# Kernel optimization log

Measured on AMD Instinct MI355X. Metric: run time of the kernel, lower is better.

Reference implementation:

```python
import jax, jax.numpy as jnp
import numpy as np
import math

D_MODEL = 512
HEADS = 8
GRID_COUNT = 40000
MAX_LEN = 5000


def _positional_embedding(d_model, max_len=MAX_LEN):
    pe = np.zeros((max_len, d_model), dtype=np.float32)
    position = np.arange(max_len, dtype=np.float32)[:, None]
    div_term = np.exp(np.arange(0, d_model, 2, dtype=np.float32) * -(math.log(10000.0) / d_model))
    pe[:, 0::2] = np.sin(position * div_term)
    pe[:, 1::2] = np.cos(position * div_term)
    return jnp.asarray(pe)  # [max_len, d_model]


def _mha(q, k, v, wq, bq, wk, bk, wv, bv, heads):
    # Faithful to SelfAttention: no 1/sqrt(d_k) scaling in the original.
    B, Sq, D = q.shape
    Sk = k.shape[1]
    dh = D // heads
    Q = (q @ wq.T + bq).reshape(B, Sq, heads, dh)
    K = (k @ wk.T + bk).reshape(B, Sk, heads, dh)
    V = (v @ wv.T + bv).reshape(B, Sk, heads, dh)
    attn = jax.nn.softmax(jnp.einsum('bqhd,bkhd->bhqk', Q, K), axis=-1)
    out = jnp.einsum('bhqk,bkhd->bqhd', attn, V)
    return out.reshape(B, Sq, D)


def setup_inputs() -> dict:
    key = jax.random.key(0)
    ks = jax.random.split(key, 20)
    B, S_CURR, S_HIST, N_MASK = 32, 128, 256, 16
    s = 1.0 / math.sqrt(D_MODEL)

    def lin(k):
        kw, kb = jax.random.split(k)
        w = jax.random.uniform(kw, (D_MODEL, D_MODEL), jnp.float32, -s, s)
        b = jax.random.uniform(kb, (D_MODEL,), jnp.float32, -s, s)
        return w, b

    h_wq, h_bq = lin(ks[0]); h_wk, h_bk = lin(ks[1]); h_wv, h_bv = lin(ks[2])
    c_wq, c_bq = lin(ks[3]); c_wk, c_bk = lin(ks[4]); c_wv, c_bv = lin(ks[5])
    x_wq, x_bq = lin(ks[6]); x_wk, x_bk = lin(ks[7]); x_wv, x_bv = lin(ks[8])
    t2_w, t2_b = lin(ks[9])
    emb = jax.random.normal(ks[10], (GRID_COUNT, D_MODEL), jnp.float32)

    return {
        'hist_traj_grid': jax.random.randint(ks[11], (B, S_HIST), 0, GRID_COUNT),
        'userId': jax.random.randint(ks[12], (B,), 0, 1000),
        'mask_pos': jax.random.randint(ks[13], (B, N_MASK), 0, S_CURR),
        'mask_curr_traj_grid': jax.random.randint(ks[14], (B, S_CURR), 0, GRID_COUNT),
        'aggregator_hist_traj_grid': jax.random.randint(ks[15], (B, S_HIST), 0, GRID_COUNT),
        'emb': emb,
        'h_wq': h_wq, 'h_bq': h_bq, 'h_wk': h_wk, 'h_bk': h_bk, 'h_wv': h_wv, 'h_bv': h_bv,
        'c_wq': c_wq, 'c_bq': c_bq, 'c_wk': c_wk, 'c_bk': c_bk, 'c_wv': c_wv, 'c_bv': c_bv,
        'x_wq': x_wq, 'x_bq': x_bq, 'x_wk': x_wk, 'x_bk': x_bk, 'x_wv': x_wv, 'x_bv': x_bv,
        't2_w': t2_w, 't2_b': t2_b,
    }


def reference(hist_traj_grid, userId, mask_pos, mask_curr_traj_grid, aggregator_hist_traj_grid,
              emb,
              h_wq, h_bq, h_wk, h_bk, h_wv, h_bv,
              c_wq, c_bq, c_wk, c_bk, c_wv, c_bv,
              x_wq, x_bq, x_wk, x_bk, x_wv, x_bv,
              t2_w, t2_b):
    pe = _positional_embedding(D_MODEL)
    hist = emb[aggregator_hist_traj_grid]          # [B, S_hist, D]
    curr = emb[mask_curr_traj_grid]                # [B, S_curr, D]
    hist = hist + pe[None, :hist.shape[1]]
    curr = curr + pe[None, :curr.shape[1]]

    hist = _mha(hist, hist, hist, h_wq, h_bq, h_wk, h_bk, h_wv, h_bv, HEADS)
    curr = _mha(curr, curr, curr, c_wq, c_bq, c_wk, c_bk, c_wv, c_bv, HEADS)
    _cross = _mha(curr, hist, hist, x_wq, x_bq, x_wk, x_bk, x_wv, x_bv, HEADS)
    # NOTE: original overwrites liner_transform output with liner_transform2(tanh(curr)),
    # so cross-attention output and liner_transform do not affect the result.
    hyb = jnp.tanh(curr) @ t2_w.T + t2_b           # [B, S_curr, D]

    # index_select of flattened [B*S, D] at mask_pos + b*S == take_along_axis over seq dim
    gathered = jnp.take_along_axis(hyb, mask_pos[:, :, None], axis=1)  # [B, n_mask, D]
    gathered = gathered.reshape(-1, D_MODEL)

    candidate = emb[2:]                            # [vocab-2, D]
    scores = gathered @ candidate.T                # [B*n_mask, vocab-2]
    return jax.nn.log_softmax(scores, axis=-1)
```

## Files before the change

kernel.cpp:

```cpp
#include <hip/hip_runtime.h>
#include <hip/hip_bf16.h>
#include <math.h>
#include <float.h>

#define B       32
#define S_CURR  128
#define D       512
#define H       8
#define DH      64
#define NM      16
#define NCAND   39998
#define MG      (B * NM)
#define SCLD    40064
#define NT      313

typedef __bf16 bf16x8_t __attribute__((ext_vector_type(8)));
typedef float  f32x4_t  __attribute__((ext_vector_type(4)));

typedef __attribute__((address_space(3))) unsigned int lds_u32_t;
typedef const __attribute__((address_space(1))) unsigned int gbl_u32_t;

__device__ __forceinline__ void async16(const void* g, void* l) {
    __builtin_amdgcn_global_load_lds((gbl_u32_t*)g, (lds_u32_t*)l, 16, 0, 0);
}

__global__ __launch_bounds__(256) void prep_kernel(
    const float* __restrict__ emb,
    const float* __restrict__ wq, const float* __restrict__ wk,
    const float* __restrict__ wv, const float* __restrict__ t2w,
    __bf16* __restrict__ embB, __bf16* __restrict__ wqB, __bf16* __restrict__ wkB,
    __bf16* __restrict__ wvB, __bf16* __restrict__ t2wB,
    const int* __restrict__ curr_idx, __bf16* __restrict__ currB,
    const int* __restrict__ mask_pos, int* __restrict__ qidx)
{
    int bx = blockIdx.x;
    if (bx < 10512) {
        const float* src; __bf16* dst; size_t n, base;
        if (bx < 10000) {
            src = emb + 2 * D; dst = embB; n = (size_t)NCAND * D; base = (size_t)bx * 2048;
        } else {
            int w = (bx - 10000) >> 7;
            base = (size_t)((bx - 10000) & 127) * 2048;
            n = (size_t)D * D;
            src = (w == 0) ? wq : (w == 1) ? wk : (w == 2) ? wv : t2w;
            dst = (w == 0) ? wqB : (w == 1) ? wkB : (w == 2) ? wvB : t2wB;
        }
        size_t i = base + (size_t)threadIdx.x * 8;
        if (i >= n) return;
        float4 a = *(const float4*)(src + i);
        float4 b = *(const float4*)(src + i + 4);
        bf16x8_t v;
        v[0] = (__bf16)a.x; v[1] = (__bf16)a.y; v[2] = (__bf16)a.z; v[3] = (__bf16)a.w;
        v[4] = (__bf16)b.x; v[5] = (__bf16)b.y; v[6] = (__bf16)b.z; v[7] = (__bf16)b.w;
        *(bf16x8_t*)(dst + i) = v;
        return;
    }
    if (bx == 14608) {
        int r = threadIdx.x;
        qidx[r] = (r >> 4) * S_CURR + mask_pos[r];
        r += 256;
        qidx[r] = (r >> 4) * S_CURR + mask_pos[r];
        return;
    }
    int bs = bx - 10512;
    int s = bs & (S_CURR - 1);
    int g = curr_idx[bs];
    const float* e = emb + (size_t)g * D;
    __bf16* o = currB + (size_t)bs * D;
    int d = threadIdx.x * 2;
    float div = expf(-(float)d * (9.210340371976184f / 512.0f));
    float ang = (float)s * div;
    o[d]     = (__bf16)(e[d]     + sinf(ang));
    o[d + 1] = (__bf16)(e[d + 1] + cosf(ang));
}

__global__ __launch_bounds__(256) void gemm_bf(
    const __bf16* __restrict__ A,
    const __bf16* __restrict__ W0, const float* __restrict__ b0, __bf16* __restrict__ C0,
    const __bf16* __restrict__ W1, const float* __restrict__ b1, __bf16* __restrict__ C1,
    const __bf16* __restrict__ W2, const float* __restrict__ b2, __bf16* __restrict__ C2,
    const int* __restrict__ rowidx)
{
    const int z = blockIdx.z;
    if (z == 2 && blockIdx.x >= 4) return;
    const __bf16* W = (z == 0) ? W0 : (z == 1) ? W1 : W2;
    const float* bias = (z == 0) ? b0 : (z == 1) ? b1 : b2;
    __bf16* C = (z == 0) ? C0 : (z == 1) ? C1 : C2;

    __shared__ __bf16 As[128 * 64];
    __shared__ __bf16 Bs[128 * 64];

    const int tid = threadIdx.x, lane = tid & 63, wave = tid >> 6;
    const int wy = wave >> 1, wx = wave & 1;
    const int m0 = blockIdx.x * 128, n0 = blockIdx.y * 128;
    const int lrow = lane >> 3;
    const int lcol = (((lane & 7) ^ lrow) & 7) * 8;

    const __bf16* aptr[4]; const __bf16* bptr[4];
#pragma unroll
    for (int i = 0; i < 4; ++i) {
        int chunk = wave * 4 + i;
        int ar = m0 + chunk * 8 + lrow;
        if (z == 2) ar = rowidx[ar];
        aptr[i] = A + (size_t)ar * 512 + lcol;
        bptr[i] = W + (size_t)(n0 + chunk * 8 + lrow) * 512 + lcol;
    }

    f32x4_t acc[4][4];
#pragma unroll
    for (int i = 0; i < 4; ++i)
#pragma unroll
        for (int j = 0; j < 4; ++j) acc[i][j] = (f32x4_t){0.f, 0.f, 0.f, 0.f};

    const int l7 = lane & 7, quad = lane >> 4, c16 = lane & 15;

    for (int kk = 0; kk < 512; kk += 64) {
#pragma unroll
        for (int i = 0; i < 4; ++i) {
            int chunk = wave * 4 + i;
            async16(aptr[i] + kk, &As[chunk * 512]);
            async16(bptr[i] + kk, &Bs[chunk * 512]);
        }
        __syncthreads();
#pragma unroll
        for (int kb = 0; kb < 2; ++kb) {
            const int goff = (((kb * 4 + quad) ^ l7)) * 8;
            bf16x8_t af[4], bfv[4];
#pragma unroll
            for (int i = 0; i < 4; ++i)
                af[i] = *(const bf16x8_t*)&As[(wy * 64 + i * 16 + c16) * 64 + goff];
#pragma unroll
            for (int j = 0; j < 4; ++j)
                bfv[j] = *(const bf16x8_t*)&Bs[(wx * 64 + j * 16 + c16) * 64 + goff];
#pragma unroll
            for (int i = 0; i < 4; ++i)
#pragma unroll
                for (int j = 0; j < 4; ++j)
                    acc[i][j] = __builtin_amdgcn_mfma_f32_16x16x32_bf16(
                        af[i], bfv[j], acc[i][j], 0, 0, 0);
        }
        __syncthreads();
    }

#pragma unroll
    for (int i = 0; i < 4; ++i)
#pragma unroll
        for (int j = 0; j < 4; ++j) {
            int col = n0 + wx * 64 + j * 16 + c16;
            float bv = bias[col];
#pragma unroll
            for (int rr = 0; rr < 4; ++rr) {
                int row = m0 + wy * 64 + i * 16 + quad * 4 + rr;
                C[(size_t)row * 512 + col] = (__bf16)(acc[i][j][rr] + bv);
            }
        }
}

__global__ __launch_bounds__(256) void gemm_scores(
    const __bf16* __restrict__ A,
    const __bf16* __restrict__ Bm,
    __bf16* __restrict__ scB,
    float* __restrict__ pmax, float* __restrict__ psum)
{
    const int bid = blockIdx.x;
    const int xcd = bid & 7, k = bid >> 3;
    const int nt = xcd * 40 + (k >> 2);
    if (nt >= NT) return;
    const int m0 = (k & 3) * 128, n0 = nt * 128;

    __shared__ __bf16 As[128 * 64];
    __shared__ __bf16 Bs[128 * 64];
    __shared__ float redm[2][128], reds[2][128];

    const int tid = threadIdx.x, lane = tid & 63, wave = tid >> 6;
    const int wy = wave >> 1, wx = wave & 1;
    const int lrow = lane >> 3;
    const int lcol = (((lane & 7) ^ lrow) & 7) * 8;

    const __bf16* aptr[4]; const __bf16* bptr[4];
#pragma unroll
    for (int i = 0; i < 4; ++i) {
        int chunk = wave * 4 + i;
        aptr[i] = A + (size_t)(m0 + chunk * 8 + lrow) * 512 + lcol;
        bptr[i] = Bm + (size_t)(n0 + chunk * 8 + lrow) * 512 + lcol;
    }

    f32x4_t acc[4][4];
#pragma unroll
    for (int i = 0; i < 4; ++i)
#pragma unroll
        for (int j = 0; j < 4; ++j) acc[i][j] = (f32x4_t){0.f, 0.f, 0.f, 0.f};

    const int l7 = lane & 7, quad = lane >> 4, c16 = lane & 15;

    for (int kk = 0; kk < 512; kk += 64) {
#pragma unroll
        for (int i = 0; i < 4; ++i) {
            int chunk = wave * 4 + i;
            async16(aptr[i] + kk, &As[chunk * 512]);
            async16(bptr[i] + kk, &Bs[chunk * 512]);
        }
        __syncthreads();
#pragma unroll
        for (int kb = 0; kb < 2; ++kb) {
            const int goff = (((kb * 4 + quad) ^ l7)) * 8;
            bf16x8_t af[4], bfv[4];
#pragma unroll
            for (int i = 0; i < 4; ++i)
                af[i] = *(const bf16x8_t*)&As[(wy * 64 + i * 16 + c16) * 64 + goff];
#pragma unroll
            for (int j = 0; j < 4; ++j)
                bfv[j] = *(const bf16x8_t*)&Bs[(wx * 64 + j * 16 + c16) * 64 + goff];
#pragma unroll
            for (int i = 0; i < 4; ++i)
#pragma unroll
                for (int j = 0; j < 4; ++j)
                    acc[i][j] = __builtin_amdgcn_mfma_f32_16x16x32_bf16(
                        af[i], bfv[j], acc[i][j], 0, 0, 0);
        }
        __syncthreads();
    }

#pragma unroll
    for (int i = 0; i < 4; ++i) {
#pragma unroll
        for (int rr = 0; rr < 4; ++rr) {
            const int row = wy * 64 + i * 16 + quad * 4 + rr;
            const size_t rowbase = (size_t)(m0 + row) * SCLD;
            float v[4]; float m = -FLT_MAX;
#pragma unroll
            for (int j = 0; j < 4; ++j) {
                int col = n0 + wx * 64 + j * 16 + c16;
                __bf16 xb = (__bf16)acc[i][j][rr];
                if (col < NCAND) {
                    scB[rowbase + col] = xb;
                    float xr = (float)xb;
                    v[j] = xr; m = fmaxf(m, xr);
                } else v[j] = -FLT_MAX;
            }
            float s = 0.f;
#pragma unroll
            for (int j = 0; j < 4; ++j)
                s += (v[j] > -FLT_MAX) ? __expf(v[j] - m) : 0.f;
#pragma unroll
            for (int mk = 1; mk < 16; mk <<= 1) {
                float om = __shfl_xor(m, mk);
                float os = __shfl_xor(s, mk);
                float mm = fmaxf(m, om);
                s = s * __expf(m - mm) + os * __expf(om - mm);
                m = mm;
            }
            if (c16 == 0) { redm[wx][row] = m; reds[wx][row] = s; }
        }
    }
    __syncthreads();
    if (tid < 128) {
        float ma = redm[0][tid], sa = reds[0][tid];
        float mb = redm[1][tid], sb = reds[1][tid];
        float mm = fmaxf(ma, mb);
        float ss = sa * __expf(ma - mm) + sb * __expf(mb - mm);
        pmax[(size_t)nt * MG + m0 + tid] = mm;
        psum[(size_t)nt * MG + m0 + tid] = ss;
    }
}

#define KPAD 72
__global__ __launch_bounds__(256) void attn_kernel(const __bf16* __restrict__ Qg,
                                                   const __bf16* __restrict__ K,
                                                   const __bf16* __restrict__ V,
                                                   __bf16* __restrict__ attnB) {
    const int b = blockIdx.x, h = blockIdx.y, t = threadIdx.x;
    __shared__ __bf16 Ks[128 * KPAD];
    __shared__ __bf16 Vs[128 * KPAD];
    __shared__ float  Qs[16 * 68];
    __shared__ float  P[16 * 130];

    for (int i = t; i < 1024; i += 256) {
        int row = i >> 3, cg = (i & 7) * 8;
        size_t gsrc = ((size_t)(b * S_CURR + row)) * D + h * DH + cg;
        *(bf16x8_t*)&Ks[row * KPAD + cg] = *(const bf16x8_t*)&K[gsrc];
        *(bf16x8_t*)&Vs[row * KPAD + cg] = *(const bf16x8_t*)&V[gsrc];
    }
    if (t < 128) {
        int q = t >> 3, cg = (t & 7) * 8;
        bf16x8_t qv = *(const bf16x8_t*)&Qg[((size_t)(b * NM + q)) * D + h * DH + cg];
#pragma unroll
        for (int u = 0; u < 8; ++u) Qs[q * 68 + cg + u] = (float)qv[u];
    }
    __syncthreads();

    const int q = t >> 4, i = t & 15;
    float sv[8];
    float lmax = -FLT_MAX;
#pragma unroll
    for (int z = 0; z < 8; ++z) {
        int kk = i + z * 16;
        float s = 0.f;
#pragma unroll
        for (int d0 = 0; d0 < DH; d0 += 8) {
            bf16x8_t kv = *(const bf16x8_t*)&Ks[kk * KPAD + d0];
#pragma unroll
            for (int u = 0; u < 8; ++u) s += Qs[q * 68 + d0 + u] * (float)kv[u];
        }
        sv[z] = s; lmax = fmaxf(lmax, s);
    }
#pragma unroll
    for (int mk = 1; mk < 16; mk <<= 1) lmax = fmaxf(lmax, __shfl_xor(lmax, mk));
    float lsum = 0.f;
#pragma unroll
    for (int z = 0; z < 8; ++z) {
        float e = __expf(sv[z] - lmax);
        P[q * 130 + i + z * 16] = e;
        lsum += e;
    }
#pragma unroll
    for (int mk = 1; mk < 16; mk <<= 1) lsum += __shfl_xor(lsum, mk);
    const float inv = 1.0f / lsum;

    const int d = i * 4;
    float a0 = 0.f, a1 = 0.f, a2 = 0.f, a3 = 0.f;
    for (int kk = 0; kk < 128; ++kk) {
        float p = P[q * 130 + kk];
        const __bf16* vr = &Vs[kk * KPAD + d];
        a0 += p * (float)vr[0]; a1 += p * (float)vr[1];
        a2 += p * (float)vr[2]; a3 += p * (float)vr[3];
    }
    __bf16* o = attnB + ((size_t)(b * NM + q)) * D + h * DH + d;
    o[0] = (__bf16)tanhf(a0 * inv); o[1] = (__bf16)tanhf(a1 * inv);
    o[2] = (__bf16)tanhf(a2 * inv); o[3] = (__bf16)tanhf(a3 * inv);
}

__global__ __launch_bounds__(256) void lse_reduce(const float* __restrict__ pmax,
                                                  const float* __restrict__ psum,
                                                  float* __restrict__ lse) {
    int row = blockIdx.x, t = threadIdx.x;
    float m = -FLT_MAX, s = 0.f;
    for (int i = t; i < NT; i += 256) {
        float om = pmax[(size_t)i * MG + row];
        float os = psum[(size_t)i * MG + row];
        float mm = fmaxf(m, om);
        s = s * __expf(m - mm) + os * __expf(om - mm);
        m = mm;
    }
    __shared__ float ms[256], ss[256];
    ms[t] = m; ss[t] = s;
    __syncthreads();
    for (int off = 128; off > 0; off >>= 1) {
        if (t < off) {
            float m1 = ms[t], s1 = ss[t], m2 = ms[t + off], s2 = ss[t + off];
            float mm = fmaxf(m1, m2);
            ms[t] = mm;
            ss[t] = s1 * __expf(m1 - mm) + s2 * __expf(m2 - mm);
        }
        __syncthreads();
    }
    if (t == 0) lse[row] = ms[0] + logf(ss[0]);
}

__global__ __launch_bounds__(256) void final_out(const __bf16* __restrict__ scB,
                                                 const float* __restrict__ lse,
                                                 float* __restrict__ out) {
    int row = blockIdx.y;
    int c0 = (blockIdx.x * 256 + threadIdx.x) * 8;
    if (c0 >= NCAND) return;
    float l = lse[row];
    bf16x8_t v = *(const bf16x8_t*)(scB + (size_t)row * SCLD + c0);
    float* o = out + (size_t)row * NCAND + c0;
    if (c0 + 8 <= NCAND) {
        *(float2*)(o)     = make_float2((float)v[0] - l, (float)v[1] - l);
        *(float2*)(o + 2) = make_float2((float)v[2] - l, (float)v[3] - l);
        *(float2*)(o + 4) = make_float2((float)v[4] - l, (float)v[5] - l);
        *(float2*)(o + 6) = make_float2((float)v[6] - l, (float)v[7] - l);
    } else {
        for (int k2 = 0; k2 < NCAND - c0; ++k2) o[k2] = (float)v[k2] - l;
    }
}

extern "C" void kernel_launch(void* const* d_in, const int* in_sizes, int n_in,
                              void* d_out, int out_size, void* d_ws, size_t ws_size,
                              hipStream_t stream) {
    const int*   mask_pos = (const int*)d_in[2];
    const int*   curr_idx = (const int*)d_in[3];
    const float* emb      = (const float*)d_in[5];
    const float* c_wq = (const float*)d_in[12];
    const float* c_bq = (const float*)d_in[13];
    const float* c_wk = (const float*)d_in[14];
    const float* c_bk = (const float*)d_in[15];
    const float* c_wv = (const float*)d_in[16];
    const float* c_bv = (const float*)d_in[17];
    const float* t2_w = (const float*)d_in[24];
    const float* t2_b = (const float*)d_in[25];
    float* out = (float*)d_out;

    char* w = (char*)d_ws;
    __bf16* embB  = (__bf16*)w;
    __bf16* scB   = (__bf16*)(w + 41025536);
    __bf16* currB = scB;
    __bf16* Kf    = (__bf16*)(w + 41025536 + 4194304);
    __bf16* Vf    = (__bf16*)(w + 41025536 + 8388608);
    __bf16* Qg    = (__bf16*)(w + 41025536 + 12582912);
    __bf16* attnB = (__bf16*)(w + 41025536 + 13107200);
    __bf16* wqB   = (__bf16*)(w + 41025536 + 13631488);
    __bf16* wkB   = (__bf16*)(w + 41025536 + 14155776);
    __bf16* wvB   = (__bf16*)(w + 41025536 + 14680064);
    __bf16* t2wB  = (__bf16*)(w + 41025536 + 15204352);
    int*    qidx  = (int*)   (w + 41025536 + 15728640);
    __bf16* gatheredB = (__bf16*)(w + 82051072);
    float*  pmax  = (float*)(w + 82575360);
    float*  psum  = (float*)(w + 83216384);
    float*  lse   = (float*)(w + 83857408);

    hipLaunchKernelGGL(prep_kernel, dim3(14609), dim3(256), 0, stream,
                       emb, c_wq, c_wk, c_wv, t2_w, embB, wqB, wkB, wvB, t2wB,
                       curr_idx, currB, mask_pos, qidx);
    hipLaunchKernelGGL(gemm_bf, dim3(32, 4, 3), dim3(256), 0, stream,
                       currB, wkB, c_bk, Kf, wvB, c_bv, Vf, wqB, c_bq, Qg, qidx);
    hipLaunchKernelGGL(attn_kernel, dim3(B, H), dim3(256), 0, stream,
                       Qg, Kf, Vf, attnB);
    hipLaunchKernelGGL(gemm_bf, dim3(4, 4, 1), dim3(256), 0, stream,
                       attnB, t2wB, t2_b, gatheredB,
                       t2wB, t2_b, gatheredB, t2wB, t2_b, gatheredB,
                       (const int*)nullptr);
    hipLaunchKernelGGL(gemm_scores, dim3(1280), dim3(256), 0, stream,
                       gatheredB, embB, scB, pmax, psum);
    hipLaunchKernelGGL(lse_reduce, dim3(MG), dim3(256), 0, stream, pmax, psum, lse);
    hipLaunchKernelGGL(final_out, dim3(20, MG), dim3(256), 0, stream, scB, lse, out);
}
```

Measured before the change: 305.6 us.

## Double-buffer GEMM LDS tiles and widen scores tile to 128x256

Both GEMM kernels now use two LDS buffers. The next K-slice is prefetched with async global-to-LDS loads while MFMAs run on the current slice, meant to hide global load latency behind compute. The scores GEMM also grows its output tile from 128x128 to 128x256, which halves the number of column tiles and the per-tile partial max/sum entries that lse_reduce has to combine. Its in-tile softmax reduction is simplified to a max-reduce followed by a sum-reduce. The trade-off is more LDS per block, more accumulator registers (launch_bounds now asks for occupancy 1) and fewer blocks to spread across the GPU.

Result: slower. 334.6 us (+9.5%).

```diff
diff --git a/kernel.cpp b/kernel.cpp
--- a/kernel.cpp
+++ b/kernel.cpp
@@ -12,7 +12,7 @@
 #define NCAND   39998
 #define MG      (B * NM)
 #define SCLD    40064
-#define NT      313
+#define NT2     157
 
 typedef __bf16 bf16x8_t __attribute__((ext_vector_type(8)));
 typedef float  f32x4_t  __attribute__((ext_vector_type(4)));
@@ -87,8 +87,8 @@
     const float* bias = (z == 0) ? b0 : (z == 1) ? b1 : b2;
     __bf16* C = (z == 0) ? C0 : (z == 1) ? C1 : C2;
 
-    __shared__ __bf16 As[128 * 64];
-    __shared__ __bf16 Bs[128 * 64];
+    __shared__ __bf16 As[2][128 * 64];
+    __shared__ __bf16 Bs[2][128 * 64];
 
     const int tid = threadIdx.x, lane = tid & 63, wave = tid >> 6;
     const int wy = wave >> 1, wx = wave & 1;
@@ -114,24 +114,35 @@
 
     const int l7 = lane & 7, quad = lane >> 4, c16 = lane & 15;
 
-    for (int kk = 0; kk < 512; kk += 64) {
-#pragma unroll
-        for (int i = 0; i < 4; ++i) {
-            int chunk = wave * 4 + i;
-            async16(aptr[i] + kk, &As[chunk * 512]);
-            async16(bptr[i] + kk, &Bs[chunk * 512]);
-        }
-        __syncthreads();
+#pragma unroll
+    for (int i = 0; i < 4; ++i) {
+        int chunk = wave * 4 + i;
+        async16(aptr[i], &As[0][chunk * 512]);
+        async16(bptr[i], &Bs[0][chunk * 512]);
+    }
+    __syncthreads();
+
+    for (int it = 0; it < 8; ++it) {
+        const int cur = it & 1;
+        if (it < 7) {
+            const int kk = (it + 1) * 64;
+#pragma unroll
+            for (int i = 0; i < 4; ++i) {
+                int chunk = wave * 4 + i;
+                async16(aptr[i] + kk, &As[cur ^ 1][chunk * 512]);
+                async16(bptr[i] + kk, &Bs[cur ^ 1][chunk * 512]);
+            }
+        }
 #pragma unroll
         for (int kb = 0; kb < 2; ++kb) {
-            const int goff = (((kb * 4 + quad) ^ l7)) * 8;
+            const int goff = ((kb * 4 + quad) ^ l7) * 8;
             bf16x8_t af[4], bfv[4];
 #pragma unroll
             for (int i = 0; i < 4; ++i)
-                af[i] = *(const bf16x8_t*)&As[(wy * 64 + i * 16 + c16) * 64 + goff];
+                af[i] = *(const bf16x8_t*)&As[cur][(wy * 64 + i * 16 + c16) * 64 + goff];
 #pragma unroll
             for (int j = 0; j < 4; ++j)
-                bfv[j] = *(const bf16x8_t*)&Bs[(wx * 64 + j * 16 + c16) * 64 + goff];
+                bfv[j] = *(const bf16x8_t*)&Bs[cur][(wx * 64 + j * 16 + c16) * 64 + goff];
 #pragma unroll
             for (int i = 0; i < 4; ++i)
 #pragma unroll
@@ -156,7 +167,7 @@
         }
 }
 
-__global__ __launch_bounds__(256) void gemm_scores(
+__global__ __launch_bounds__(256, 1) void gemm_scores(
     const __bf16* __restrict__ A,
     const __bf16* __restrict__ Bm,
     __bf16* __restrict__ scB,
@@ -164,57 +175,66 @@
 {
     const int bid = blockIdx.x;
     const int xcd = bid & 7, k = bid >> 3;
-    const int nt = xcd * 40 + (k >> 2);
-    if (nt >= NT) return;
-    const int m0 = (k & 3) * 128, n0 = nt * 128;
-
-    __shared__ __bf16 As[128 * 64];
-    __shared__ __bf16 Bs[128 * 64];
+    const int n2 = xcd * 20 + (k >> 2);
+    if (n2 >= NT2) return;
+    const int m0 = (k & 3) * 128, n0 = n2 * 256;
+
+    __shared__ __bf16 As[2][128 * 64];
+    __shared__ __bf16 Bs[2][256 * 64];
     __shared__ float redm[2][128], reds[2][128];
 
     const int tid = threadIdx.x, lane = tid & 63, wave = tid >> 6;
-    const int wy = wave >> 1, wx = wave & 1;
+    const int wy = wave & 1, wx = wave >> 1;
     const int lrow = lane >> 3;
     const int lcol = (((lane & 7) ^ lrow) & 7) * 8;
 
-    const __bf16* aptr[4]; const __bf16* bptr[4];
-#pragma unroll
-    for (int i = 0; i < 4; ++i) {
-        int chunk = wave * 4 + i;
-        aptr[i] = A + (size_t)(m0 + chunk * 8 + lrow) * 512 + lcol;
-        bptr[i] = Bm + (size_t)(n0 + chunk * 8 + lrow) * 512 + lcol;
-    }
-
-    f32x4_t acc[4][4];
+    const __bf16* aptr[4]; const __bf16* bptr[8];
 #pragma unroll
     for (int i = 0; i < 4; ++i)
-#pragma unroll
-        for (int j = 0; j < 4; ++j) acc[i][j] = (f32x4_t){0.f, 0.f, 0.f, 0.f};
+        aptr[i] = A + (size_t)(m0 + (wave * 4 + i) * 8 + lrow) * 512 + lcol;
+#pragma unroll
+    for (int i = 0; i < 8; ++i)
+        bptr[i] = Bm + (size_t)(n0 + (wave * 8 + i) * 8 + lrow) * 512 + lcol;
+
+    f32x4_t acc[4][8];
+#pragma unroll
+    for (int i = 0; i < 4; ++i)
+#pragma unroll
+        for (int j = 0; j < 8; ++j) acc[i][j] = (f32x4_t){0.f, 0.f, 0.f, 0.f};
 
     const int l7 = lane & 7, quad = lane >> 4, c16 = lane & 15;
 
-    for (int kk = 0; kk < 512; kk += 64) {
-#pragma unroll
-        for (int i = 0; i < 4; ++i) {
-            int chunk = wave * 4 + i;
-            async16(aptr[i] + kk, &As[chunk * 512]);
-            async16(bptr[i] + kk, &Bs[chunk * 512]);
-        }
-        __syncthreads();
+#pragma unroll
+    for (int i = 0; i < 4; ++i) async16(aptr[i], &As[0][(wave * 4 + i) * 512]);
+#pragma unroll
+    for (int i = 0; i < 8; ++i) async16(bptr[i], &Bs[0][(wave * 8 + i) * 512]);
+    __syncthreads();
+
+    for (int it = 0; it < 8; ++it) {
+        const int cur = it & 1;
+        if (it < 7) {
+            const int kk = (it + 1) * 64;
+#pragma unroll
+            for (int i = 0; i < 4; ++i)
+                async16(aptr[i] + kk, &As[cur ^ 1][(wave * 4 + i) * 512]);
+#pragma unroll
+            for (int i = 0; i < 8; ++i)
+                async16(bptr[i] + kk, &Bs[cur ^ 1][(wave * 8 + i) * 512]);
+        }
 #pragma unroll
         for (int kb = 0; kb < 2; ++kb) {
-            const int goff = (((kb * 4 + quad) ^ l7)) * 8;
-            bf16x8_t af[4], bfv[4];
+            const int goff = ((kb * 4 + quad) ^ l7) * 8;
+            bf16x8_t af[4], bfv[8];
 #pragma unroll
             for (int i = 0; i < 4; ++i)
-                af[i] = *(const bf16x8_t*)&As[(wy * 64 + i * 16 + c16) * 64 + goff];
-#pragma unroll
-            for (int j = 0; j < 4; ++j)
-                bfv[j] = *(const bf16x8_t*)&Bs[(wx * 64 + j * 16 + c16) * 64 + goff];
+                af[i] = *(const bf16x8_t*)&As[cur][(wy * 64 + i * 16 + c16) * 64 + goff];
+#pragma unroll
+            for (int j = 0; j < 8; ++j)
+                bfv[j] = *(const bf16x8_t*)&Bs[cur][(wx * 128 + j * 16 + c16) * 64 + goff];
 #pragma unroll
             for (int i = 0; i < 4; ++i)
 #pragma unroll
-                for (int j = 0; j < 4; ++j)
+                for (int j = 0; j < 8; ++j)
                     acc[i][j] = __builtin_amdgcn_mfma_f32_16x16x32_bf16(
                         af[i], bfv[j], acc[i][j], 0, 0, 0);
         }
@@ -227,29 +247,26 @@
         for (int rr = 0; rr < 4; ++rr) {
             const int row = wy * 64 + i * 16 + quad * 4 + rr;
             const size_t rowbase = (size_t)(m0 + row) * SCLD;
-            float v[4]; float m = -FLT_MAX;
-#pragma unroll
-            for (int j = 0; j < 4; ++j) {
-                int col = n0 + wx * 64 + j * 16 + c16;
+            float v[8]; float m = -FLT_MAX;
+#pragma unroll
+            for (int j = 0; j < 8; ++j) {
+                int col = n0 + wx * 128 + j * 16 + c16;
                 __bf16 xb = (__bf16)acc[i][j][rr];
                 if (col < NCAND) {
                     scB[rowbase + col] = xb;
-                    float xr = (float)xb;
-                    v[j] = xr; m = fmaxf(m, xr);
+                    v[j] = (float)xb; m = fmaxf(m, v[j]);
                 } else v[j] = -FLT_MAX;
             }
+#pragma unroll
+            for (int mk = 1; mk < 16; mk <<= 1)
+                m = fmaxf(m, __shfl_xor(m, mk));
             float s = 0.f;
 #pragma unroll
-            for (int j = 0; j < 4; ++j)
-                s += (v[j] > -FLT_MAX) ? __expf(v[j] - m) : 0.f;
-#pragma unroll
-            for (int mk = 1; mk < 16; mk <<= 1) {
-                float om = __shfl_xor(m, mk);
-                float os = __shfl_xor(s, mk);
-                float mm = fmaxf(m, om);
-                s = s * __expf(m - mm) + os * __expf(om - mm);
-                m = mm;
-            }
+            for (int j = 0; j < 8; ++j)
+                if (v[j] > -FLT_MAX) s += __expf(v[j] - m);
+#pragma unroll
+            for (int mk = 1; mk < 16; mk <<= 1)
+                s += __shfl_xor(s, mk);
             if (c16 == 0) { redm[wx][row] = m; reds[wx][row] = s; }
         }
     }
@@ -259,8 +276,8 @@
         float mb = redm[1][tid], sb = reds[1][tid];
         float mm = fmaxf(ma, mb);
         float ss = sa * __expf(ma - mm) + sb * __expf(mb - mm);
-        pmax[(size_t)nt * MG + m0 + tid] = mm;
-        psum[(size_t)nt * MG + m0 + tid] = ss;
+        pmax[(size_t)n2 * MG + m0 + tid] = mm;
+        psum[(size_t)n2 * MG + m0 + tid] = ss;
     }
 }
 
@@ -335,7 +352,7 @@
                                                   float* __restrict__ lse) {
     int row = blockIdx.x, t = threadIdx.x;
     float m = -FLT_MAX, s = 0.f;
-    for (int i = t; i < NT; i += 256) {
+    for (int i = t; i < NT2; i += 256) {
         float om = pmax[(size_t)i * MG + row];
         float os = psum[(size_t)i * MG + row];
         float mm = fmaxf(m, om);
@@ -350,7 +367,7 @@
             float m1 = ms[t], s1 = ss[t], m2 = ms[t + off], s2 = ss[t + off];
             float mm = fmaxf(m1, m2);
             ms[t] = mm;
-            ss[t] = s1 * __expf(m1 - mm) + s2 * __expf(m2 - mm);
+            ss[t] = (s1 * __expf(m1 - mm)) + (s2 * __expf(m2 - mm));
         }
         __syncthreads();
     }
@@ -421,7 +438,7 @@
                        attnB, t2wB, t2_b, gatheredB,
                        t2wB, t2_b, gatheredB, t2wB, t2_b, gatheredB,
                        (const int*)nullptr);
-    hipLaunchKernelGGL(gemm_scores, dim3(1280), dim3(256), 0, stream,
+    hipLaunchKernelGGL(gemm_scores, dim3(640), dim3(256), 0, stream,
                        gatheredB, embB, scB, pmax, psum);
     hipLaunchKernelGGL(lse_reduce, dim3(MG), dim3(256), 0, stream, pmax, psum, lse);
     hipLaunchKernelGGL(final_out, dim3(20, MG), dim3(256), 0, stream, scB, lse, out);
```
